# Kernel tuning notes

Hardware: AMD Instinct MI355X
Metric: run time of the kernel (lower is better)

Reference implementation:

```python
import jax, jax.numpy as jnp
import numpy as np

EPS = 0.1  # eps added to covariance sums, as in torch cov()
N, D, N_CLASSES = 4096, 1024, 64


def setup_inputs() -> dict:
    key = jax.random.key(0)
    k1, k2 = jax.random.split(key)
    inputs = jax.random.normal(k1, (N, D), dtype=jnp.float32)
    targets = jax.random.randint(k2, (N,), 0, N_CLASSES, dtype=jnp.int32)
    return {"inputs": inputs, "targets": targets}


def _masked_sqdiff_sum(M, x):
    # Per-dim sum over masked pairs (i,j) of (x_i - x_j)^2, without
    # materializing the [n, n, d] difference tensor:
    #   sum_ij M_ij (x_id^2 + x_jd^2 - 2 x_id x_jd)
    row = M.sum(axis=1)  # [n]
    col = M.sum(axis=0)  # [n]
    x2 = x * x
    return row @ x2 + col @ x2 - 2.0 * jnp.sum(x * (M @ x), axis=0)  # [d]


def _jeffrey_loss(inputs, targets):
    n = inputs.shape[0]
    same = targets[:, None] == targets[None, :]
    eye = jnp.eye(n, dtype=bool)
    pos_m = (same & ~eye).astype(inputs.dtype)  # positive pairs, i != j
    neg_m = (~same).astype(inputs.dtype)        # negative pairs

    # Covariances are computed on detached diffs in the torch code
    xd = jax.lax.stop_gradient(inputs)
    cnt_pos = pos_m.sum()
    cnt_neg = neg_m.sum()
    sigma1 = (_masked_sqdiff_sum(pos_m, xd) + EPS) / cnt_pos  # [d]
    sigma0 = (_masked_sqdiff_sum(neg_m, xd) + EPS) / cnt_neg  # [d]
    weights = 1.0 / sigma0 - 1.0 / sigma1  # [d], constant w.r.t. grad

    # S[i, j] = sum_d weights_d * (x_i - x_j)_d^2, via gram expansion
    xw = inputs * weights            # [n, d]
    sq = jnp.sum(inputs * xw, axis=1)  # [n], sum_d w_d x_d^2
    S = sq[:, None] + sq[None, :] - 2.0 * inputs @ xw.T  # [n, n]

    # BCEWithLogitsLoss(mean): label 1 on positive pairs (logits a),
    # label 0 on negative pairs (logits b)
    loss_sum = jnp.sum(pos_m * jax.nn.softplus(-S)) + jnp.sum(neg_m * jax.nn.softplus(S))
    return loss_sum / (cnt_pos + cnt_neg)


def reference(inputs, targets):
    return _jeffrey_loss(inputs, targets)
```

## Files before the change

### kernel.cpp

```cpp
#include <hip/hip_runtime.h>
#include <stdint.h>

#define N_ROWS 4096
#define DIM    1024
#define NCLS   64
#define EPSV   0.1f

typedef __attribute__((ext_vector_type(4))) float f32x4;

__device__ __forceinline__ void async_cp16(const void* g, void* l) {
    __builtin_amdgcn_global_load_lds((const __attribute__((address_space(1))) void*)g,
                                     (__attribute__((address_space(3))) void*)l,
                                     16, 0, 0);
}

__device__ __forceinline__ float softplus(float x) {
    return fmaxf(x, 0.f) + __logf(1.f + __expf(-fabsf(x)));
}

__global__ __launch_bounds__(256) void k_cstats(const float* __restrict__ X,
                                                const int* __restrict__ tgt,
                                                float* __restrict__ csumR,
                                                float* __restrict__ csqR) {
    __shared__ int rows[N_ROWS];
    __shared__ int nrows_s;
    int tid = threadIdx.x;
    int c = blockIdx.x >> 2, q = blockIdx.x & 3;
    if (tid == 0) nrows_s = 0;
    __syncthreads();
    for (int i = tid; i < N_ROWS; i += 256)
        if (tgt[i] == c) { int p = atomicAdd(&nrows_s, 1); rows[p] = i; }
    __syncthreads();
    int n = nrows_s;
    int d = q * 256 + tid;
    float s = 0.f, qq = 0.f;
    #pragma unroll 4
    for (int r = 0; r < n; r++) {
        float x = X[(size_t)rows[r] * DIM + d];
        s += x; qq += x * x;
    }
    csumR[c * DIM + d] = s;
    csqR [c * DIM + d] = qq;
}

__global__ __launch_bounds__(128) void k_weights(const int* __restrict__ tgt,
                                                 const float* __restrict__ csumR,
                                                 const float* __restrict__ csqR,
                                                 float* __restrict__ w,
                                                 float* __restrict__ scal,
                                                 float* __restrict__ loss_out) {
    __shared__ int hist[NCLS];
    __shared__ float redw[2];
    int tid = threadIdx.x, b = blockIdx.x;
    if (tid < NCLS) hist[tid] = 0;
    __syncthreads();
    for (int i = tid; i < N_ROWS; i += 128) atomicAdd(&hist[tgt[i]], 1);
    __syncthreads();
    long long sp = 0, ss = 0;
    for (int c = 0; c < NCLS; c++) { long long cc = hist[c]; sp += cc * (cc - 1); ss += cc * cc; }
    float cnt_pos = (float)sp;
    float cnt_neg = (float)((long long)N_ROWS * N_ROWS - ss);
    int d = b * 128 + tid;
    float A = 0.f, X2 = 0.f, T = 0.f, SS = 0.f;
    #pragma unroll 8
    for (int c = 0; c < NCLS; c++) {
        float s = csumR[c * DIM + d];
        float q = csqR [c * DIM + d];
        A += (float)hist[c] * q; X2 += q; T += s; SS += s * s;
    }
    float posnum = 2.f * (A - SS);
    float negnum = 2.f * ((float)N_ROWS * X2 - A - T * T + SS);
    float wd = cnt_neg / (negnum + EPSV) - cnt_pos / (posnum + EPSV);
    w[d] = wd;
    float m = wd * wd;
    for (int off = 32; off; off >>= 1) m += __shfl_down(m, off, 64);
    int wv = tid >> 6, ln = tid & 63;
    if (ln == 0) redw[wv] = m;
    __syncthreads();
    if (b == 0 && tid == 0) {
        float ms = (redw[0] + redw[1]) / 128.f;
        scal[0] = exp2f(roundf(log2f(sqrtf(ms) + 1e-30f)));
        loss_out[0] = 0.0f;
    }
}

__global__ __launch_bounds__(256) void k_prep(const float* __restrict__ X,
                                              const float* __restrict__ w,
                                              const float* __restrict__ scal,
                                              unsigned int* __restrict__ Xb8,
                                              unsigned int* __restrict__ XWb8,
                                              float* __restrict__ sq) {
    int row = blockIdx.x, tid = threadIdx.x;
    float inv_sw = 1.0f / scal[0];
    float4 x  = ((const float4*)(X + (size_t)row * DIM))[tid];
    float4 ww = ((const float4*)w)[tid];
    float4 xw = make_float4(x.x * ww.x, x.y * ww.y, x.z * ww.z, x.w * ww.w);
    float p = x.x * xw.x + x.y * xw.y + x.z * xw.z + x.w * xw.w;
    unsigned ux = __builtin_amdgcn_cvt_pk_fp8_f32(x.x, x.y, 0, false);
    ux = __builtin_amdgcn_cvt_pk_fp8_f32(x.z, x.w, ux, true);
    unsigned uw = __builtin_amdgcn_cvt_pk_fp8_f32(xw.x * inv_sw, xw.y * inv_sw, 0, false);
    uw = __builtin_amdgcn_cvt_pk_fp8_f32(xw.z * inv_sw, xw.w * inv_sw, uw, true);
    int t = tid >> 3, qd = (tid >> 1) & 3, o = tid & 1;
    int s = (row >> 2) & 3;
    int widx = row * 256 + t * 8 + (qd ^ s) * 2 + o;
    Xb8 [widx] = ux;
    XWb8[widx] = uw;
    for (int off = 32; off; off >>= 1) p += __shfl_down(p, off, 64);
    __shared__ float red[4];
    int wv = tid >> 6, ln = tid & 63;
    if (ln == 0) red[wv] = p;
    __syncthreads();
    if (tid == 0) sq[row] = red[0] + red[1] + red[2] + red[3];
}

__global__ __launch_bounds__(512, 4) void k_gemm_loss(const unsigned char* __restrict__ Xb8,
                                                      const unsigned char* __restrict__ XWb8,
                                                      const float* __restrict__ sq,
                                                      const int* __restrict__ tgt,
                                                      const float* __restrict__ scal,
                                                      float* __restrict__ loss) {
    __shared__ __align__(16) unsigned char As[6][4096];
    __shared__ __align__(16) unsigned char Bs[6][4096];
    __shared__ float sqI[128], sqJ[128];
    __shared__ int   tIs[128], tJs[128];
    __shared__ float red[8];

    int tid = threadIdx.x;
    int wave = tid >> 6, lane = tid & 63;

    int g = blockIdx.x & 7, s = blockIdx.x >> 3;
    int j0 = g, j1 = 15 - g, j2 = 16 + g;
    int n0 = j0 + 1, n1 = j1 + 1, n2 = j2 + 1;
    int jt, it;
    if      (s < n0)           { jt = j0; it = s; }
    else if (s < n0 + n1)      { jt = j1; it = s - n0; }
    else if (s < n0 + n1 + n2) { jt = j2; it = s - n0 - n1; }
    else                       { jt = 31 - g; it = s - n0 - n1 - n2; }

    bool isA = wave < 4;
    const unsigned char* srcb = (isA ? Xb8 : XWb8) + (size_t)((isA ? it : jt) * 128) * DIM;
    unsigned char* slab = isA ? &As[0][0] : &Bs[0][0];
    int ch = (wave & 3) * 64 + lane;
    int r = ch >> 1, h = ch & 1;
    const unsigned char* gp = srcb + (size_t)r * DIM + h * 16;
    unsigned char* lb = slab + (wave & 3) * 1024;

    int lr = lane & 15, kq = lane >> 4;
    int offA[4], offB[2];
    int wrow = (wave >> 2) * 64, wcol = (wave & 3) * 32;
    #pragma unroll
    for (int mi = 0; mi < 4; mi++) {
        int row = wrow + mi * 16 + lr;
        offA[mi] = row * 32 + (kq ^ ((row >> 2) & 3)) * 8;
    }
    #pragma unroll
    for (int nj = 0; nj < 2; nj++) {
        int col = wcol + nj * 16 + lr;
        offB[nj] = col * 32 + (kq ^ ((col >> 2) & 3)) * 8;
    }

    f32x4 acc[4][2];
    #pragma unroll
    for (int i = 0; i < 4; i++)
        #pragma unroll
        for (int j = 0; j < 2; j++) acc[i][j] = (f32x4){0.f, 0.f, 0.f, 0.f};

    #pragma unroll
    for (int st = 0; st < 4; st++) async_cp16(gp + st * 32, lb + st * 4096);

    for (int p = 0; p < 16; p++) {
        if (p < 15) asm volatile("s_waitcnt vmcnt(2)" ::: "memory");
        else        asm volatile("s_waitcnt vmcnt(0)" ::: "memory");
        asm volatile("s_barrier" ::: "memory");
        if (p < 14) {
            int s0 = 2 * p + 4;
            async_cp16(gp + (size_t)s0 * 32, lb + (s0 % 6) * 4096);
            async_cp16(gp + (size_t)(s0 + 1) * 32, lb + ((s0 + 1) % 6) * 4096);
        }
        #pragma unroll
        for (int t = 0; t < 2; t++) {
            int bufi = (2 * p + t) % 6;
            const unsigned char* Ab = As[bufi];
            const unsigned char* Bb = Bs[bufi];
            long long av[4], bv[2];
            #pragma unroll
            for (int i = 0; i < 4; i++) av[i] = *(const long long*)(Ab + offA[i]);
            #pragma unroll
            for (int j = 0; j < 2; j++) bv[j] = *(const long long*)(Bb + offB[j]);
            #pragma unroll
            for (int i = 0; i < 4; i++)
                #pragma unroll
                for (int j = 0; j < 2; j++)
                    acc[i][j] = __builtin_amdgcn_mfma_f32_16x16x32_fp8_fp8(av[i], bv[j], acc[i][j], 0, 0, 0);
        }
    }

    __syncthreads();
    if (tid < 128)      { sqI[tid] = sq[it * 128 + tid]; tIs[tid] = tgt[it * 128 + tid]; }
    else if (tid < 256) { int u = tid - 128; sqJ[u] = sq[jt * 128 + u]; tJs[u] = tgt[jt * 128 + u]; }
    __syncthreads();

    float sw2 = 2.0f * scal[0];
    float sum = 0.f;
    bool diagTile = (it == jt);
    #pragma unroll
    for (int j = 0; j < 2; j++) {
        int col = wcol + j * 16 + (lane & 15);
        float sj = sqJ[col]; int tj = tJs[col];
        #pragma unroll
        for (int i = 0; i < 4; i++) {
            int rbase = wrow + i * 16 + (lane >> 4) * 4;
            #pragma unroll
            for (int rr = 0; rr < 4; rr++) {
                int rowp = rbase + rr;
                float S = sqI[rowp] + sj - sw2 * acc[i][j][rr];
                float v;
                if (tIs[rowp] == tj) v = (diagTile && rowp == col) ? 0.f : softplus(-S);
                else                 v = softplus(S);
                sum += v;
            }
        }
    }
    float scale = (diagTile ? 1.f : 2.f) * (1.f / ((float)N_ROWS * (float)(N_ROWS - 1)));
    sum *= scale;
    for (int off = 32; off; off >>= 1) sum += __shfl_down(sum, off, 64);
    if (lane == 0) red[wave] = sum;
    __syncthreads();
    if (tid == 0) {
        float t = 0.f;
        #pragma unroll
        for (int wv = 0; wv < 8; wv++) t += red[wv];
        atomicAdd(loss, t);
    }
}

extern "C" void kernel_launch(void* const* d_in, const int* in_sizes, int n_in,
                              void* d_out, int out_size, void* d_ws, size_t ws_size,
                              hipStream_t stream) {
    const float* X  = (const float*)d_in[0];
    const int* tgt  = (const int*)d_in[1];
    float* out = (float*)d_out;
    char* ws = (char*)d_ws;
    const size_t MB = 1u << 20;

    float* w      = (float*)ws;
    float* sq     = (float*)(ws + 4096);
    float* scal   = (float*)(ws + 24576);
    unsigned int* Xb8  = (unsigned int*)(ws + 1 * MB);
    unsigned int* XWb8 = (unsigned int*)(ws + 5 * MB);
    float* csumR  = (float*)(ws + 9 * MB);
    float* csqR   = (float*)(ws + 9 * MB + 256 * 1024);

    k_cstats  <<<256,  256, 0, stream>>>(X, tgt, csumR, csqR);
    k_weights <<<8,    128, 0, stream>>>(tgt, csumR, csqR, w, scal, out);
    k_prep    <<<4096, 256, 0, stream>>>(X, w, scal, Xb8, XWb8, sq);
    k_gemm_loss<<<528, 512, 0, stream>>>((const unsigned char*)Xb8, (const unsigned char*)XWb8,
                                         sq, tgt, scal, out);
}
```

Measured before the change: 117.8 us.

## Switch GEMM to 16x16x128 scaled FP8 MFMA with 256-thread blocks

Replaces the 16x16x32 fp8 MFMA with the gfx950 scaled 16x16x128 f8f6f4 MFMA, which consumes a 128-byte K slice per step. The block shrinks to 4 waves, each computing a 64x64 subtile. The LDS layout changes to a 128-byte-row XOR swizzle applied at load time, and k_prep now writes rows linearly. The six-stage async pipeline becomes a single-buffered load, wait, compute loop over 8 K-steps, so fewer instructions are issued but loads no longer overlap with MFMA work inside a block.

```diff
diff --git a/kernel.cpp b/kernel.cpp
--- a/kernel.cpp
+++ b/kernel.cpp
@@ -7,6 +7,8 @@
 #define EPSV   0.1f
 
 typedef __attribute__((ext_vector_type(4))) float f32x4;
+typedef __attribute__((ext_vector_type(4))) int   i32x4;
+typedef __attribute__((ext_vector_type(8))) int   i32x8;
 
 __device__ __forceinline__ void async_cp16(const void* g, void* l) {
     __builtin_amdgcn_global_load_lds((const __attribute__((address_space(1))) void*)g,
@@ -100,9 +102,7 @@
     ux = __builtin_amdgcn_cvt_pk_fp8_f32(x.z, x.w, ux, true);
     unsigned uw = __builtin_amdgcn_cvt_pk_fp8_f32(xw.x * inv_sw, xw.y * inv_sw, 0, false);
     uw = __builtin_amdgcn_cvt_pk_fp8_f32(xw.z * inv_sw, xw.w * inv_sw, uw, true);
-    int t = tid >> 3, qd = (tid >> 1) & 3, o = tid & 1;
-    int s = (row >> 2) & 3;
-    int widx = row * 256 + t * 8 + (qd ^ s) * 2 + o;
+    int widx = row * 256 + tid;
     Xb8 [widx] = ux;
     XWb8[widx] = uw;
     for (int off = 32; off; off >>= 1) p += __shfl_down(p, off, 64);
@@ -113,17 +113,17 @@
     if (tid == 0) sq[row] = red[0] + red[1] + red[2] + red[3];
 }
 
-__global__ __launch_bounds__(512, 4) void k_gemm_loss(const unsigned char* __restrict__ Xb8,
+__global__ __launch_bounds__(256, 3) void k_gemm_loss(const unsigned char* __restrict__ Xb8,
                                                       const unsigned char* __restrict__ XWb8,
                                                       const float* __restrict__ sq,
                                                       const int* __restrict__ tgt,
                                                       const float* __restrict__ scal,
                                                       float* __restrict__ loss) {
-    __shared__ __align__(16) unsigned char As[6][4096];
-    __shared__ __align__(16) unsigned char Bs[6][4096];
+    __shared__ __align__(16) unsigned char As[16384];
+    __shared__ __align__(16) unsigned char Bs[16384];
     __shared__ float sqI[128], sqJ[128];
     __shared__ int   tIs[128], tJs[128];
-    __shared__ float red[8];
+    __shared__ float red[4];
 
     int tid = threadIdx.x;
     int wave = tid >> 6, lane = tid & 63;
@@ -137,74 +137,79 @@
     else if (s < n0 + n1 + n2) { jt = j2; it = s - n0 - n1; }
     else                       { jt = 31 - g; it = s - n0 - n1 - n2; }
 
-    bool isA = wave < 4;
-    const unsigned char* srcb = (isA ? Xb8 : XWb8) + (size_t)((isA ? it : jt) * 128) * DIM;
-    unsigned char* slab = isA ? &As[0][0] : &Bs[0][0];
-    int ch = (wave & 3) * 64 + lane;
-    int r = ch >> 1, h = ch & 1;
-    const unsigned char* gp = srcb + (size_t)r * DIM + h * 16;
-    unsigned char* lb = slab + (wave & 3) * 1024;
-
-    int lr = lane & 15, kq = lane >> 4;
-    int offA[4], offB[2];
-    int wrow = (wave >> 2) * 64, wcol = (wave & 3) * 32;
+    const unsigned char* Abase = Xb8  + (size_t)(it * 128) * DIM;
+    const unsigned char* Bbase = XWb8 + (size_t)(jt * 128) * DIM;
+    const unsigned char* gpA[4];
+    const unsigned char* gpB[4];
+    int ldo[4];
+    #pragma unroll
+    for (int i = 0; i < 4; i++) {
+        int r  = (wave * 4 + i) * 8 + (lane >> 3);
+        int pg = lane & 7;
+        size_t off = (size_t)r * DIM + (size_t)((pg ^ (r & 7)) << 4);
+        gpA[i] = Abase + off;
+        gpB[i] = Bbase + off;
+        ldo[i] = (wave * 4 + i) * 1024;
+    }
+
+    int lr = lane & 15, hk = lane >> 4;
+    int wrow = (wave >> 1) * 64, wcol = (wave & 1) * 64;
+    int offA[4], offB[4];
     #pragma unroll
     for (int mi = 0; mi < 4; mi++) {
-        int row = wrow + mi * 16 + lr;
-        offA[mi] = row * 32 + (kq ^ ((row >> 2) & 3)) * 8;
-    }
-    #pragma unroll
-    for (int nj = 0; nj < 2; nj++) {
-        int col = wcol + nj * 16 + lr;
-        offB[nj] = col * 32 + (kq ^ ((col >> 2) & 3)) * 8;
-    }
-
-    f32x4 acc[4][2];
+        int r = wrow + mi * 16 + lr;
+        offA[mi] = r * 128 + (((hk * 2) ^ (r & 7)) << 4);
+    }
+    #pragma unroll
+    for (int nj = 0; nj < 4; nj++) {
+        int c = wcol + nj * 16 + lr;
+        offB[nj] = c * 128 + (((hk * 2) ^ (c & 7)) << 4);
+    }
+
+    f32x4 acc[4][4];
     #pragma unroll
     for (int i = 0; i < 4; i++)
         #pragma unroll
-        for (int j = 0; j < 2; j++) acc[i][j] = (f32x4){0.f, 0.f, 0.f, 0.f};
-
-    #pragma unroll
-    for (int st = 0; st < 4; st++) async_cp16(gp + st * 32, lb + st * 4096);
-
-    for (int p = 0; p < 16; p++) {
-        if (p < 15) asm volatile("s_waitcnt vmcnt(2)" ::: "memory");
-        else        asm volatile("s_waitcnt vmcnt(0)" ::: "memory");
-        asm volatile("s_barrier" ::: "memory");
-        if (p < 14) {
-            int s0 = 2 * p + 4;
-            async_cp16(gp + (size_t)s0 * 32, lb + (s0 % 6) * 4096);
-            async_cp16(gp + (size_t)(s0 + 1) * 32, lb + ((s0 + 1) % 6) * 4096);
+        for (int j = 0; j < 4; j++) acc[i][j] = (f32x4){0.f, 0.f, 0.f, 0.f};
+
+    for (int st = 0; st < 8; st++) {
+        __syncthreads();
+        #pragma unroll
+        for (int i = 0; i < 4; i++) async_cp16(gpA[i] + st * 128, As + ldo[i]);
+        #pragma unroll
+        for (int i = 0; i < 4; i++) async_cp16(gpB[i] + st * 128, Bs + ldo[i]);
+        asm volatile("s_waitcnt vmcnt(0)" ::: "memory");
+        __syncthreads();
+
+        i32x8 bv[4];
+        #pragma unroll
+        for (int nj = 0; nj < 4; nj++) {
+            i32x4 lo = *(const i32x4*)(Bs + offB[nj]);
+            i32x4 hi = *(const i32x4*)(Bs + (offB[nj] ^ 16));
+            bv[nj] = __builtin_shufflevector(lo, hi, 0, 1, 2, 3, 4, 5, 6, 7);
         }
         #pragma unroll
-        for (int t = 0; t < 2; t++) {
-            int bufi = (2 * p + t) % 6;
-            const unsigned char* Ab = As[bufi];
-            const unsigned char* Bb = Bs[bufi];
-            long long av[4], bv[2];
+        for (int mi = 0; mi < 4; mi++) {
+            i32x4 lo = *(const i32x4*)(As + offA[mi]);
+            i32x4 hi = *(const i32x4*)(As + (offA[mi] ^ 16));
+            i32x8 av = __builtin_shufflevector(lo, hi, 0, 1, 2, 3, 4, 5, 6, 7);
             #pragma unroll
-            for (int i = 0; i < 4; i++) av[i] = *(const long long*)(Ab + offA[i]);
-            #pragma unroll
-            for (int j = 0; j < 2; j++) bv[j] = *(const long long*)(Bb + offB[j]);
-            #pragma unroll
-            for (int i = 0; i < 4; i++)
-                #pragma unroll
-                for (int j = 0; j < 2; j++)
-                    acc[i][j] = __builtin_amdgcn_mfma_f32_16x16x32_fp8_fp8(av[i], bv[j], acc[i][j], 0, 0, 0);
+            for (int nj = 0; nj < 4; nj++)
+                acc[mi][nj] = __builtin_amdgcn_mfma_scale_f32_16x16x128_f8f6f4(
+                    av, bv[nj], acc[mi][nj], 0, 0, 0, 127, 0, 127);
         }
     }
 
     __syncthreads();
     if (tid < 128)      { sqI[tid] = sq[it * 128 + tid]; tIs[tid] = tgt[it * 128 + tid]; }
-    else if (tid < 256) { int u = tid - 128; sqJ[u] = sq[jt * 128 + u]; tJs[u] = tgt[jt * 128 + u]; }
+    else                { int u = tid - 128; sqJ[u] = sq[jt * 128 + u]; tJs[u] = tgt[jt * 128 + u]; }
     __syncthreads();
 
     float sw2 = 2.0f * scal[0];
     float sum = 0.f;
     bool diagTile = (it == jt);
     #pragma unroll
-    for (int j = 0; j < 2; j++) {
+    for (int j = 0; j < 4; j++) {
         int col = wcol + j * 16 + (lane & 15);
         float sj = sqJ[col]; int tj = tJs[col];
         #pragma unroll
@@ -227,9 +232,7 @@
     if (lane == 0) red[wave] = sum;
     __syncthreads();
     if (tid == 0) {
-        float t = 0.f;
-        #pragma unroll
-        for (int wv = 0; wv < 8; wv++) t += red[wv];
+        float t = red[0] + red[1] + red[2] + red[3];
         atomicAdd(loss, t);
     }
 }
@@ -254,6 +257,6 @@
     k_cstats  <<<256,  256, 0, stream>>>(X, tgt, csumR, csqR);
     k_weights <<<8,    128, 0, stream>>>(tgt, csumR, csqR, w, scal, out);
     k_prep    <<<4096, 256, 0, stream>>>(X, w, scal, Xb8, XWb8, sq);
-    k_gemm_loss<<<528, 512, 0, stream>>>((const unsigned char*)Xb8, (const unsigned char*)XWb8,
+    k_gemm_loss<<<528, 256, 0, stream>>>((const unsigned char*)Xb8, (const unsigned char*)XWb8,
                                          sq, tgt, scal, out);
 }
```

After: 288.3 us. 145% more time.
